# Performance work log

Hardware: AMD Instinct MI355X
Metric: run time of the kernel (lower is better)

The kernel has to match this reference:

```python
import jax, jax.numpy as jnp
import numpy as np

TEMPERATURE = 1.0
CHUNK = 128  # node-block size for the curvature pass


def setup_inputs() -> dict:
    key = jax.random.key(0)
    k1, k2 = jax.random.split(key)
    N, D = 4096, 64
    x = jax.random.normal(k1, (N, D), dtype=jnp.float32)
    # sparse binary adjacency (avg degree ~16) + ring so min degree >= 2
    A = (jax.random.uniform(k2, (N, N)) < 0.004).astype(jnp.float32)
    i = jnp.arange(N)
    A = A.at[i, i].set(0.0)
    A = A.at[i, (i + 1) % N].set(1.0)
    A = A.at[(i + 1) % N, i].set(1.0)
    return {"node_embeddings": x, "adj_matrix": A}


def _physics_components(x, A):
    N, d = x.shape
    mask = A > 0
    deg = jnp.sum(A, axis=-1)                      # [N]

    # ---- total energy ----
    kinetic = jnp.sum(x * x, axis=-1)
    nb = A @ x                                     # neighbor aggregate [N,d]
    potential = -jnp.sum(x * nb, axis=-1)
    total_energy = kinetic + potential / (deg + 1e-8)

    # ---- local entropy over neighbor similarities ----
    xn = x / jnp.maximum(jnp.linalg.norm(x, axis=-1, keepdims=True), 1e-12)
    S = xn @ xn.T                                  # cosine sims [N,N]
    logits = jnp.where(mask, S / TEMPERATURE, -1e30)
    P = jax.nn.softmax(logits, axis=-1)            # masked softmax per row
    local_entropy = -jnp.sum(jnp.where(mask, P * jnp.log(P + 1e-8), 0.0), axis=-1)

    # ---- equilibrium deviation (5-NN local mean in embedding space) ----
    sq = jnp.sum(x * x, axis=-1)
    D2 = jnp.maximum(sq[:, None] + sq[None, :] - 2.0 * (x @ x.T), 1e-12)
    dist = jnp.sqrt(D2)                            # [N,N]
    _, idx = jax.lax.top_k(-dist, 6)               # smallest 6 (self first)
    local_means = jnp.mean(x[idx[:, 1:]], axis=1)  # [N,d]
    gdev = jnp.linalg.norm(x - jnp.mean(x, axis=0, keepdims=True), axis=-1)
    ldev = jnp.linalg.norm(x - local_means, axis=-1)
    equilibrium_deviation = 0.6 * gdev + 0.4 * ldev

    # ---- structural centrality ----
    en = jnp.linalg.norm(x, axis=-1)
    structural_centrality = 0.5 * deg / (N - 1) + 0.5 * en / jnp.max(en)

    # ---- information flow: unbiased var of neighbor sims ----
    ms = jnp.sum(jnp.where(mask, S, 0.0), axis=-1) / deg
    information_flow = jnp.sum(jnp.where(mask, (S - ms[:, None]) ** 2, 0.0), axis=-1) / (deg - 1.0)

    # ---- stability: 1/(1 + mean unbiased var of neighbor embeddings) ----
    m1 = nb / deg[:, None]
    ex2 = A @ (x * x)
    var_dim = (ex2 - deg[:, None] * m1 * m1) / (deg - 1.0)[:, None]
    stability = 1.0 / (1.0 + jnp.mean(var_dim, axis=-1))

    # ---- discrete curvature: 1 - mean pairwise cos angle of centered neighbors ----
    # mean_{j<k} u_j.u_k = (||sum u||^2 - sum ||u||^2) / (deg*(deg-1))
    def body(_, ids):
        xb = x[ids]                                 # [B,d]
        mb = mask[ids]                              # [B,N]
        c = x[None, :, :] - xb[:, None, :]          # [B,N,d]
        nrm = jnp.sqrt(jnp.maximum(jnp.sum(c * c, -1), 1e-12))
        u = jnp.where(mb[..., None], c / jnp.maximum(nrm, 1e-8)[..., None], 0.0)
        s = jnp.sum(u, axis=1)                      # [B,d]
        ssq = jnp.sum(u * u, axis=(1, 2))           # [B]
        db = jnp.sum(mb.astype(x.dtype), axis=-1)
        mean_cos = (jnp.sum(s * s, -1) - ssq) / (db * (db - 1.0))
        return None, 1.0 - mean_cos

    _, curv = jax.lax.scan(body, None, jnp.arange(N).reshape(-1, CHUNK))
    graph_curvature = curv.reshape(N)

    return (total_energy, local_entropy, equilibrium_deviation,
            structural_centrality, information_flow, stability, graph_curvature)


def reference(node_embeddings, adj_matrix):
    return _physics_components(node_embeddings, adj_matrix)
```

## Files before the change

kernel.cpp:

```cpp
#include <hip/hip_runtime.h>
#include <math.h>

#define NN 4096
#define DD 64
#define NSPLIT 64
#define JW 64

typedef _Float16 half8 __attribute__((ext_vector_type(8)));
typedef float f32x4 __attribute__((ext_vector_type(4)));

__device__ __forceinline__ unsigned sxu(unsigned v, int o){
  return (unsigned)__shfl_xor((int)v, o, 64);
}
__device__ __forceinline__ unsigned umn(unsigned a, unsigned b){ return a<b?a:b; }
__device__ __forceinline__ unsigned umx(unsigned a, unsigned b){ return a<b?b:a; }
__device__ __forceinline__ unsigned med3u(unsigned a, unsigned b, unsigned c){
  unsigned r; asm("v_med3_u32 %0, %1, %2, %3" : "=v"(r) : "v"(a), "v"(b), "v"(c)); return r;
}
__device__ __forceinline__ unsigned min3u(unsigned a, unsigned b, unsigned c){
  unsigned r; asm("v_min3_u32 %0, %1, %2, %3" : "=v"(r) : "v"(a), "v"(b), "v"(c)); return r;
}

__device__ __forceinline__ unsigned packkey32(float m, int j){
  float q = fmaf(m, 2048.f, 524288.f);
  q = fminf(fmaxf(q, 0.f), 1048575.f);
  return (((unsigned)q) << 12) | (unsigned)j;
}

__device__ __forceinline__ void ins5u(unsigned k, unsigned b[5]){
  unsigned nb0 = umn(k, b[0]);
  b[4] = med3u(k, b[3], b[4]);
  b[3] = med3u(k, b[2], b[3]);
  b[2] = med3u(k, b[1], b[2]);
  b[1] = med3u(k, b[0], b[1]);
  b[0] = nb0;
}

__device__ __forceinline__ void mergeStage32(unsigned b[5], int st){
  unsigned p0=sxu(b[0],st),p1=sxu(b[1],st),p2=sxu(b[2],st),p3=sxu(b[3],st),p4=sxu(b[4],st);
  unsigned o0=umn(b[0],p0);
  unsigned o1=min3u(b[1],p1, umx(b[0],p0));
  unsigned o2=min3u(b[2],p2, umn(umx(b[0],p1),umx(b[1],p0)));
  unsigned o3=min3u(b[3],p3, min3u(umx(b[0],p2), umx(b[1],p1), umx(b[2],p0)));
  unsigned o4=min3u(b[4],p4, umn(umn(umx(b[0],p3),umx(b[1],p2)),
                                 umn(umx(b[2],p1),umx(b[3],p0))));
  b[0]=o0;b[1]=o1;b[2]=o2;b[3]=o3;b[4]=o4;
}

__device__ __forceinline__ void mergeLocal32(const unsigned a[5], const unsigned c[5], unsigned b[5]){
  b[0]=umn(a[0],c[0]);
  b[1]=min3u(a[1],c[1], umx(a[0],c[0]));
  b[2]=min3u(a[2],c[2], umn(umx(a[0],c[1]),umx(a[1],c[0])));
  b[3]=min3u(a[3],c[3], min3u(umx(a[0],c[2]), umx(a[1],c[1]), umx(a[2],c[0])));
  b[4]=min3u(a[4],c[4], umn(umn(umx(a[0],c[3]),umx(a[1],c[2])),
                            umn(umx(a[2],c[1]),umx(a[3],c[0]))));
}

__global__ __launch_bounds__(256) void k_prec(const float* __restrict__ x,
                      float* __restrict__ sq,
                      _Float16* __restrict__ xh, _Float16* __restrict__ xl,
                      float* __restrict__ msum_part, float* __restrict__ maxsq_part){
  __shared__ float part[4][64];
  __shared__ float mxp[4];
  const int w = threadIdx.x>>6, lane = threadIdx.x&63;
  const int n0 = blockIdx.x*16 + w*4;
  float v0 = x[(size_t)(n0+0)*DD + lane];
  float v1 = x[(size_t)(n0+1)*DD + lane];
  float v2 = x[(size_t)(n0+2)*DD + lane];
  float v3 = x[(size_t)(n0+3)*DD + lane];
  float s0=v0*v0, s1=v1*v1, s2=v2*v2, s3=v3*v3;
#pragma unroll
  for(int o=1;o<64;o<<=1){
    s0 += __shfl_xor(s0,o,64); s1 += __shfl_xor(s1,o,64);
    s2 += __shfl_xor(s2,o,64); s3 += __shfl_xor(s3,o,64);
  }
  float vv[4] = {v0,v1,v2,v3};
  float ss[4] = {s0,s1,s2,s3};
#pragma unroll
  for(int q=0;q<4;q++){
    float v = vv[q];
    _Float16 h = (_Float16)v;
    _Float16 l = (_Float16)(v - (float)h);
    xh[(size_t)(n0+q)*DD+lane] = h;
    xl[(size_t)(n0+q)*DD+lane] = l;
    if(lane==0) sq[n0+q]=ss[q];
  }
  if(lane==0) mxp[w] = fmaxf(fmaxf(s0,s1), fmaxf(s2,s3));
  part[w][lane] = v0+v1+v2+v3; __syncthreads();
  if(w==0){
    msum_part[blockIdx.x*64 + lane] = part[0][lane]+part[1][lane]+part[2][lane]+part[3][lane];
    if(lane==0) maxsq_part[blockIdx.x] = fmaxf(fmaxf(mxp[0],mxp[1]), fmaxf(mxp[2],mxp[3]));
  }
}

__device__ __forceinline__ f32x4 gram6(const half8 J[4],
    half8 Ih0, half8 Ih1, half8 Il0, half8 Il1){
  const f32x4 z = {0.f,0.f,0.f,0.f};
  f32x4 a1 = __builtin_amdgcn_mfma_f32_16x16x32_f16(J[0], Ih0, z, 0,0,0);
  f32x4 a2 = __builtin_amdgcn_mfma_f32_16x16x32_f16(J[2], Ih0, z, 0,0,0);
  a1 = __builtin_amdgcn_mfma_f32_16x16x32_f16(J[1], Ih1, a1, 0,0,0);
  a2 = __builtin_amdgcn_mfma_f32_16x16x32_f16(J[3], Ih1, a2, 0,0,0);
  a1 = __builtin_amdgcn_mfma_f32_16x16x32_f16(J[0], Il0, a1, 0,0,0);
  a1 = __builtin_amdgcn_mfma_f32_16x16x32_f16(J[1], Il1, a1, 0,0,0);
  return a1 + a2;
}

__global__ __launch_bounds__(256, 4) void k_mega(
    const float* __restrict__ x, const float* __restrict__ A,
    const float* __restrict__ sq,
    const _Float16* __restrict__ xh, const _Float16* __restrict__ xl,
    unsigned* __restrict__ cand,
    const float* __restrict__ msum_part, const float* __restrict__ maxsq_part,
    float* __restrict__ msum, float* __restrict__ max_sq, float* __restrict__ deg_out,
    float* __restrict__ o_te, float* __restrict__ o_ent,
    float* __restrict__ o_if, float* __restrict__ o_st, float* __restrict__ o_cv)
{
  __shared__ __align__(16) char smem[16384];
  const int bid = blockIdx.x;
  const int tid = threadIdx.x;
  const int w = tid>>6, lane = tid&63;

  if(bid == 0){
    float* rr = (float*)smem;
    float* rm = (float*)(smem + 1024);
    float s = 0.f;
    for(int p=w; p<256; p+=4) s += msum_part[p*64 + lane];
    rr[w*64 + lane] = s;
    float m = maxsq_part[w*64 + lane];
#pragma unroll
    for(int o=1;o<64;o<<=1) m = fmaxf(m, __shfl_xor(m,o,64));
    if(lane==0) rm[w] = m;
    __syncthreads();
    if(w==0){
      msum[lane] = rr[0*64+lane]+rr[1*64+lane]+rr[2*64+lane]+rr[3*64+lane];
      if(lane==0) max_sq[0] = fmaxf(fmaxf(rm[0],rm[1]), fmaxf(rm[2],rm[3]));
    }
    return;
  }

  const int t = bid - 1;
  if(t % 5 == 0){
    int*   nbrw  = (int*)smem + w*128;
    float* Svalw = (float*)(smem + 2048) + w*128;
    const int i = (t/5)*4 + w;
    const float xid = x[(size_t)i*DD + lane];
    const float sqi = sq[i];
    const float eni = sqrtf(sqi);
    const float4* A4 = (const float4*)(A + (size_t)i*NN);
    const unsigned long long below = (1ull << lane) - 1ull;

    int base = 0;
#define COMPACT(VAL, JJ) { \
    bool p_ = (VAL) > 0.f; \
    unsigned long long m_ = __ballot(p_); \
    int ofs_ = base + (int)__popcll(m_ & below); \
    if(p_ && ofs_ < 128) nbrw[ofs_] = (JJ); \
    base += (int)__popcll(m_); \
  }
    for(int ch=0; ch<4; ++ch){
      float4 av[4];
#pragma unroll
      for(int qq=0; qq<4; ++qq) av[qq] = A4[lane + 64*(ch*4+qq)];
#pragma unroll
      for(int qq=0; qq<4; ++qq){
        int jb = 4*(lane + 64*(ch*4+qq));
        COMPACT(av[qq].x, jb+0);
        COMPACT(av[qq].y, jb+1);
        COMPACT(av[qq].z, jb+2);
        COMPACT(av[qq].w, jb+3);
      }
    }
#undef COMPACT
    const int deg = base;

    const float degf = (float)deg;
    const int dmax = min(deg, 128);
    float nb_d=0.f, ex2_d=0.f, s_d=0.f, ssq=0.f;

    for(int c0=0; c0<dmax; c0+=8){
      int jq[8]; float aq[8], qq[8];
#pragma unroll
      for(int q=0;q<8;q++) jq[q] = nbrw[min(c0+q, dmax-1)];
#pragma unroll
      for(int q=0;q<8;q++) aq[q] = x[(size_t)jq[q]*DD + lane];
#pragma unroll
      for(int q=0;q<8;q++) qq[q] = sq[jq[q]];
      asm volatile("" :: "v"(aq[0]), "v"(aq[1]), "v"(aq[2]), "v"(aq[3]),
                         "v"(aq[4]), "v"(aq[5]), "v"(aq[6]), "v"(aq[7]));
      float p[8];
#pragma unroll
      for(int q=0;q<8;q++) p[q] = xid*aq[q];
#pragma unroll
      for(int o=1;o<64;o<<=1){
#pragma unroll
        for(int q=0;q<8;q++) p[q] += __shfl_xor(p[q],o,64);
      }
#pragma unroll
      for(int q=0;q<8;q++){
        const bool valid = (c0+q) < deg;
        float c2 = fmaxf(sqi + qq[q] - 2.0f*p[q], 1e-12f);
        float inv = 1.0f/fmaxf(sqrtf(c2), 1e-8f);
        nb_d  += valid ? aq[q] : 0.f;
        ex2_d += valid ? aq[q]*aq[q] : 0.f;
        s_d   += valid ? (aq[q]-xid)*inv : 0.f;
        ssq   += valid ? c2*inv*inv : 0.f;
        if(valid && lane==q) Svalw[c0+q] = p[q]/(eni*sqrtf(qq[q]));
      }
    }

    float t0 = xid*nb_d;
    float m1 = nb_d/degf;
    float t1 = (ex2_d - degf*m1*m1)/(degf-1.0f);
    float t2 = s_d*s_d;
    float t3 = 0.f, t4 = 0.f;
    for(int s=lane; s<dmax; s+=64){ float v=Svalw[s]; t3 += expf(v); t4 += v; }
#pragma unroll
    for(int o=1;o<64;o<<=1){
      t0 += __shfl_xor(t0,o,64); t1 += __shfl_xor(t1,o,64); t2 += __shfl_xor(t2,o,64);
      t3 += __shfl_xor(t3,o,64); t4 += __shfl_xor(t4,o,64);
    }
    const float pot = t0, varm = t1*(1.0f/DD), s2 = t2, se = t3, ms = t4/degf;

    float e0=0.f, e1=0.f;
    const float inv_se = 1.0f/se;
    for(int s=lane; s<dmax; s+=64){
      float v = Svalw[s];
      float pp = expf(v)*inv_se;
      e0 -= pp*logf(pp + 1e-8f);
      float dv = v-ms; e1 += dv*dv;
    }
#pragma unroll
    for(int o=1;o<64;o<<=1){ e0 += __shfl_xor(e0,o,64); e1 += __shfl_xor(e1,o,64); }

    if(lane==0){
      o_te[i]  = sqi - pot/(degf + 1e-8f);
      o_ent[i] = e0;
      o_if[i]  = e1/(degf-1.0f);
      o_st[i]  = 1.0f/(1.0f + varm);
      o_cv[i]  = 1.0f - (s2 - ssq)/(degf*(degf-1.0f));
      deg_out[i] = degf;
    }
  } else {
    _Float16* jHi = (_Float16*)smem;
    _Float16* jLo = (_Float16*)(smem + 8192);
    const int kid = (t/5)*4 + (t%5) - 1;
    const int split = kid & (NSPLIT-1);
    const int strip = (kid >> 6)*4 + w;
    const int ibase = strip*16, j0 = split*JW;
    const int col = lane & 15, kg = lane >> 4;
    const int vo = col*DD + kg*8;
    const int myi = ibase + col;

#pragma unroll
    for(int q_=0;q_<2;q_++){
      int g_ = q_*256 + tid;
      int r_ = g_ >> 3;
      int c_ = (g_ & 7) ^ (r_ & 7);
      const _Float16* sH_ = xh + (size_t)(j0 + r_)*DD + c_*8;
      const _Float16* sL_ = xl + (size_t)(j0 + r_)*DD + c_*8;
      __builtin_amdgcn_global_load_lds(
        (const __attribute__((address_space(1))) unsigned int*)sH_,
        (__attribute__((address_space(3))) unsigned int*)(jHi + g_*8), 16, 0, 0);
      __builtin_amdgcn_global_load_lds(
        (const __attribute__((address_space(1))) unsigned int*)sL_,
        (__attribute__((address_space(3))) unsigned int*)(jLo + g_*8), 16, 0, 0);
    }

    const _Float16* pih = xh + (size_t)ibase*DD + vo;
    const _Float16* pil = xl + (size_t)ibase*DD + vo;
    const half8 Ih0 = *(const half8*)(pih);
    const half8 Ih1 = *(const half8*)(pih+32);
    const half8 Il0 = *(const half8*)(pil);
    const half8 Il1 = *(const half8*)(pil+32);

    const int jb0 = j0 + kg*4;
    float4 sq0 = *(const float4*)(sq + jb0);
    float4 sq1 = *(const float4*)(sq + jb0 + 16);
    float4 sq2 = *(const float4*)(sq + jb0 + 32);
    float4 sq3 = *(const float4*)(sq + jb0 + 48);

    unsigned bA[5], bB[5];
#pragma unroll
    for(int k=0;k<5;k++){ bA[k]=0xFFFFFFFFu; bB[k]=0xFFFFFFFFu; }

    __syncthreads();

    half8 JT[4];
#define TILE(TT, SQV, LIST) { \
    const int rl_ = (TT)*16 + col; \
    const int sw_ = rl_ & 7; \
    JT[0] = *(const half8*)(jHi + (rl_*8 + ( kg      ^ sw_))*8); \
    JT[1] = *(const half8*)(jHi + (rl_*8 + ((kg + 4) ^ sw_))*8); \
    JT[2] = *(const half8*)(jLo + (rl_*8 + ( kg      ^ sw_))*8); \
    JT[3] = *(const half8*)(jLo + (rl_*8 + ((kg + 4) ^ sw_))*8); \
    f32x4 d_ = gram6(JT, Ih0, Ih1, Il0, Il1); \
    float sv_[4] = {SQV.x, SQV.y, SQV.z, SQV.w}; \
    const int jt0_ = jb0 + (TT)*16; \
    _Pragma("unroll") \
    for(int r_=0;r_<4;r_++){ \
      unsigned kk_ = packkey32(fmaf(-2.0f, d_[r_], sv_[r_]), jt0_+r_); \
      kk_ = (jt0_+r_==myi) ? 0xFFFFFFFFu : kk_; \
      ins5u(kk_, LIST); \
    } }

    TILE(0, sq0, bA);
    TILE(1, sq1, bB);
    TILE(2, sq2, bA);
    TILE(3, sq3, bB);
#undef TILE

    unsigned b[5];
    mergeLocal32(bA, bB, b);
    mergeStage32(b, 16);
    mergeStage32(b, 32);

    if(kg==0){
#pragma unroll
      for(int k=0;k<5;k++)
        cand[((size_t)myi*NSPLIT + split)*5 + k] = b[k];
    }
  }
}

__global__ __launch_bounds__(256) void k_nnsel(
    const float* __restrict__ x, const unsigned* __restrict__ cand,
    const float* __restrict__ msum, const float* __restrict__ max_sq,
    const float* __restrict__ deg, const float* __restrict__ sq,
    float* __restrict__ o_eq, float* __restrict__ o_sc)
{
  const int w = threadIdx.x>>6, l = threadIdx.x&63;
  const int i = blockIdx.x*4 + w;
  const unsigned* cr = cand + (size_t)i*(NSPLIT*5);
  unsigned c0 = cr[l], c1 = cr[64+l], c2 = cr[128+l], c3 = cr[192+l], c4 = cr[256+l];

  int sel[5];
#pragma unroll
  for(int k=0;k<5;k++){
    unsigned d = umn(min3u(c0,c1,c2), umn(c3,c4));
#pragma unroll
    for(int o=1;o<64;o<<=1) d = umn(d, sxu(d,o));
    sel[k] = (int)(d & 0xFFFu);
    if(c0==d) c0=0xFFFFFFFFu;
    else if(c1==d) c1=0xFFFFFFFFu;
    else if(c2==d) c2=0xFFFFFFFFu;
    else if(c3==d) c3=0xFFFFFFFFu;
    else if(c4==d) c4=0xFFFFFFFFu;
  }

  float smv=0.f;
#pragma unroll
  for(int k=0;k<5;k++) smv += x[(size_t)sel[k]*DD + l];
  float xiv = x[(size_t)i*DD + l];
  float lv = xiv - smv*0.2f;
  float gv = xiv - msum[l]*(1.0f/NN);
  float pl = lv*lv, pg = gv*gv;
#pragma unroll
  for(int o=1;o<64;o<<=1){ pl += __shfl_xor(pl,o,64); pg += __shfl_xor(pg,o,64); }
  if(l==0){
    o_eq[i] = 0.6f*sqrtf(pg) + 0.4f*sqrtf(pl);
    o_sc[i] = 0.5f*deg[i]/(float)(NN-1) + 0.5f*sqrtf(sq[i])/sqrtf(max_sq[0]);
  }
}

extern "C" void kernel_launch(void* const* d_in, const int* in_sizes, int n_in,
                              void* d_out, int out_size, void* d_ws, size_t ws_size,
                              hipStream_t stream) {
  const float* x = (const float*)d_in[0];
  const float* A = (const float*)d_in[1];
  float* out = (float*)d_out;
  float* ws  = (float*)d_ws;
  float*     sq        = ws;
  float*     msum      = ws + 4096;
  float*     max_sq    = ws + 4160;
  float*     deg       = ws + 4224;
  float*     msum_part = ws + 8320;
  float*     maxsq_part= ws + 24704;
  _Float16*  xh        = (_Float16*)(ws + 24960);
  _Float16*  xl        = (_Float16*)(ws + 156032);
  unsigned*  cand      = (unsigned*)(ws + 287104);

  k_prec<<<NN/16, 256, 0, stream>>>(x, sq, xh, xl, msum_part, maxsq_part);
  k_mega<<<5*NN/4 + 1, 256, 0, stream>>>(x, A, sq, xh, xl, cand,
                                         msum_part, maxsq_part, msum, max_sq, deg,
                                         out, out+NN, out+4*NN, out+5*NN, out+6*NN);
  k_nnsel<<<NN/4, 256, 0, stream>>>(x, cand, msum, max_sq, deg, sq,
                                    out+2*NN, out+3*NN);
}
```

Before: 56.80 us.

## Process two row strips per wave in kNN blocks to reuse staged j-tile

Each kNN block now computes distances for two 16-row strips per wave against the same LDS-staged 64-column j tile. This halves the number of kNN blocks and the global-to-LDS staging traffic per useful work, so the mega kernel grid shrinks from 5N/4 to 3N/4 blocks. The cost is more registers per thread for the second strip's operands and its top-5 list, plus a reshuffled block interleave between the graph-row and kNN work.

```diff
diff --git a/kernel.cpp b/kernel.cpp
--- a/kernel.cpp
+++ b/kernel.cpp
@@ -45,15 +45,6 @@
   unsigned o4=min3u(b[4],p4, umn(umn(umx(b[0],p3),umx(b[1],p2)),
                                  umn(umx(b[2],p1),umx(b[3],p0))));
   b[0]=o0;b[1]=o1;b[2]=o2;b[3]=o3;b[4]=o4;
-}
-
-__device__ __forceinline__ void mergeLocal32(const unsigned a[5], const unsigned c[5], unsigned b[5]){
-  b[0]=umn(a[0],c[0]);
-  b[1]=min3u(a[1],c[1], umx(a[0],c[0]));
-  b[2]=min3u(a[2],c[2], umn(umx(a[0],c[1]),umx(a[1],c[0])));
-  b[3]=min3u(a[3],c[3], min3u(umx(a[0],c[2]), umx(a[1],c[1]), umx(a[2],c[0])));
-  b[4]=min3u(a[4],c[4], umn(umn(umx(a[0],c[3]),umx(a[1],c[2])),
-                            umn(umx(a[2],c[1]),umx(a[3],c[0]))));
 }
 
 __global__ __launch_bounds__(256) void k_prec(const float* __restrict__ x,
@@ -139,10 +130,10 @@
   }
 
   const int t = bid - 1;
-  if(t % 5 == 0){
+  if(t % 3 == 0){
     int*   nbrw  = (int*)smem + w*128;
     float* Svalw = (float*)(smem + 2048) + w*128;
-    const int i = (t/5)*4 + w;
+    const int i = (t/3)*4 + w;
     const float xid = x[(size_t)i*DD + lane];
     const float sqi = sq[i];
     const float eni = sqrtf(sqi);
@@ -243,13 +234,15 @@
   } else {
     _Float16* jHi = (_Float16*)smem;
     _Float16* jLo = (_Float16*)(smem + 8192);
-    const int kid = (t/5)*4 + (t%5) - 1;
+    const int kid = (t/3)*2 + (t%3) - 1;
     const int split = kid & (NSPLIT-1);
-    const int strip = (kid >> 6)*4 + w;
-    const int ibase = strip*16, j0 = split*JW;
+    const int sg = kid >> 6;
+    const int stripA = sg*8 + w, stripB = sg*8 + w + 4;
+    const int ibaseA = stripA*16, ibaseB = stripB*16;
+    const int j0 = split*JW;
     const int col = lane & 15, kg = lane >> 4;
     const int vo = col*DD + kg*8;
-    const int myi = ibase + col;
+    const int myiA = ibaseA + col, myiB = ibaseB + col;
 
 #pragma unroll
     for(int q_=0;q_<2;q_++){
@@ -266,12 +259,18 @@
         (__attribute__((address_space(3))) unsigned int*)(jLo + g_*8), 16, 0, 0);
     }
 
-    const _Float16* pih = xh + (size_t)ibase*DD + vo;
-    const _Float16* pil = xl + (size_t)ibase*DD + vo;
-    const half8 Ih0 = *(const half8*)(pih);
-    const half8 Ih1 = *(const half8*)(pih+32);
-    const half8 Il0 = *(const half8*)(pil);
-    const half8 Il1 = *(const half8*)(pil+32);
+    const _Float16* pihA = xh + (size_t)ibaseA*DD + vo;
+    const _Float16* pilA = xl + (size_t)ibaseA*DD + vo;
+    const half8 IhA0 = *(const half8*)(pihA);
+    const half8 IhA1 = *(const half8*)(pihA+32);
+    const half8 IlA0 = *(const half8*)(pilA);
+    const half8 IlA1 = *(const half8*)(pilA+32);
+    const _Float16* pihB = xh + (size_t)ibaseB*DD + vo;
+    const _Float16* pilB = xl + (size_t)ibaseB*DD + vo;
+    const half8 IhB0 = *(const half8*)(pihB);
+    const half8 IhB1 = *(const half8*)(pihB+32);
+    const half8 IlB0 = *(const half8*)(pilB);
+    const half8 IlB1 = *(const half8*)(pilB+32);
 
     const int jb0 = j0 + kg*4;
     float4 sq0 = *(const float4*)(sq + jb0);
@@ -286,38 +285,44 @@
     __syncthreads();
 
     half8 JT[4];
-#define TILE(TT, SQV, LIST) { \
+#define TILE(TT, SQV) { \
     const int rl_ = (TT)*16 + col; \
     const int sw_ = rl_ & 7; \
     JT[0] = *(const half8*)(jHi + (rl_*8 + ( kg      ^ sw_))*8); \
     JT[1] = *(const half8*)(jHi + (rl_*8 + ((kg + 4) ^ sw_))*8); \
     JT[2] = *(const half8*)(jLo + (rl_*8 + ( kg      ^ sw_))*8); \
     JT[3] = *(const half8*)(jLo + (rl_*8 + ((kg + 4) ^ sw_))*8); \
-    f32x4 d_ = gram6(JT, Ih0, Ih1, Il0, Il1); \
+    f32x4 dA_ = gram6(JT, IhA0, IhA1, IlA0, IlA1); \
+    f32x4 dB_ = gram6(JT, IhB0, IhB1, IlB0, IlB1); \
     float sv_[4] = {SQV.x, SQV.y, SQV.z, SQV.w}; \
     const int jt0_ = jb0 + (TT)*16; \
     _Pragma("unroll") \
     for(int r_=0;r_<4;r_++){ \
-      unsigned kk_ = packkey32(fmaf(-2.0f, d_[r_], sv_[r_]), jt0_+r_); \
-      kk_ = (jt0_+r_==myi) ? 0xFFFFFFFFu : kk_; \
-      ins5u(kk_, LIST); \
+      unsigned kA_ = packkey32(fmaf(-2.0f, dA_[r_], sv_[r_]), jt0_+r_); \
+      kA_ = (jt0_+r_==myiA) ? 0xFFFFFFFFu : kA_; \
+      ins5u(kA_, bA); \
+      unsigned kB_ = packkey32(fmaf(-2.0f, dB_[r_], sv_[r_]), jt0_+r_); \
+      kB_ = (jt0_+r_==myiB) ? 0xFFFFFFFFu : kB_; \
+      ins5u(kB_, bB); \
     } }
 
-    TILE(0, sq0, bA);
-    TILE(1, sq1, bB);
-    TILE(2, sq2, bA);
-    TILE(3, sq3, bB);
+    TILE(0, sq0);
+    TILE(1, sq1);
+    TILE(2, sq2);
+    TILE(3, sq3);
 #undef TILE
 
-    unsigned b[5];
-    mergeLocal32(bA, bB, b);
-    mergeStage32(b, 16);
-    mergeStage32(b, 32);
+    mergeStage32(bA, 16);
+    mergeStage32(bA, 32);
+    mergeStage32(bB, 16);
+    mergeStage32(bB, 32);
 
     if(kg==0){
 #pragma unroll
-      for(int k=0;k<5;k++)
-        cand[((size_t)myi*NSPLIT + split)*5 + k] = b[k];
+      for(int k=0;k<5;k++){
+        cand[((size_t)myiA*NSPLIT + split)*5 + k] = bA[k];
+        cand[((size_t)myiB*NSPLIT + split)*5 + k] = bB[k];
+      }
     }
   }
 }
@@ -380,7 +385,7 @@
   unsigned*  cand      = (unsigned*)(ws + 287104);
 
   k_prec<<<NN/16, 256, 0, stream>>>(x, sq, xh, xl, msum_part, maxsq_part);
-  k_mega<<<5*NN/4 + 1, 256, 0, stream>>>(x, A, sq, xh, xl, cand,
+  k_mega<<<3*NN/4 + 1, 256, 0, stream>>>(x, A, sq, xh, xl, cand,
                                          msum_part, maxsq_part, msum, max_sq, deg,
                                          out, out+NN, out+4*NN, out+5*NN, out+6*NN);
   k_nnsel<<<NN/4, 256, 0, stream>>>(x, cand, msum, max_sq, deg, sq,
```

After: 56.57 us. Within noise of the previous version (-0.4%).
